# Optimization experiments

Hardware: AMD Instinct MI355X
Metric: run time of the kernel (lower is better)

The kernel has to match this reference:

```python
import jax, jax.numpy as jnp
import numpy as np

D = 1024      # input_dim / embed_dim
H = 1024      # hidden_dim
H2 = H // 2
M = 15        # n_masks
NH = 4        # n_heads
B = 8192
LN_EPS = 1e-5


def setup_inputs() -> dict:
    key = jax.random.key(0)
    ks = jax.random.split(key, 16)
    s = 0.02
    return {
        "x": jax.random.normal(ks[0], (B, D), jnp.float32),
        # nn.MultiheadAttention params (torch layout: y = x @ W.T + b)
        "in_proj_w": jax.random.normal(ks[1], (3 * D, D), jnp.float32) * s,
        "in_proj_b": jax.random.normal(ks[2], (3 * D,), jnp.float32) * s,
        "out_proj_w": jax.random.normal(ks[3], (D, D), jnp.float32) * s,
        "out_proj_b": jax.random.normal(ks[4], (D,), jnp.float32) * s,
        # 15 mask MLPs stacked along leading axis (grouped GEMM form)
        "W1": jax.random.normal(ks[5], (M, D, H), jnp.float32) * s,
        "b1": jax.random.normal(ks[6], (M, H), jnp.float32) * s,
        "ln_g": jnp.ones((M, H), jnp.float32),
        "ln_b": jnp.zeros((M, H), jnp.float32),
        "W2": jax.random.normal(ks[7], (M, H, H2), jnp.float32) * s,
        "b2": jax.random.normal(ks[8], (M, H2), jnp.float32) * s,
        "W3": jax.random.normal(ks[9], (M, H2, D), jnp.float32) * s,
        "b3": jax.random.normal(ks[10], (M, D), jnp.float32) * s,
    }


def reference(x, in_proj_w, in_proj_b, out_proj_w, out_proj_b,
              W1, b1, ln_g, ln_b, W2, b2, W3, b3):
    Bn = x.shape[0]
    hd = D // NH
    # --- seq_len=1 self-attention ---
    qkv = x @ in_proj_w.T + in_proj_b                      # [B, 3D]
    q, k, v = jnp.split(qkv, 3, axis=-1)                   # each [B, D]
    qh = q.reshape(Bn, NH, hd)
    kh = k.reshape(Bn, NH, hd)
    vh = v.reshape(Bn, NH, hd)
    scores = jnp.sum(qh * kh, axis=-1) / jnp.sqrt(jnp.float32(hd))  # [B, NH]
    # softmax over kv length = 1 -> all ones (kept for faithfulness)
    w = jax.nn.softmax(scores[..., None], axis=-1)         # [B, NH, 1]
    attn = (w * vh).reshape(Bn, D)                         # [B, D]
    a = attn @ out_proj_w.T + out_proj_b                   # [B, D]
    # --- 15 mask MLPs as one grouped GEMM stack (Dropout is eval->identity) ---
    h1 = jnp.einsum('bd,mdh->mbh', a, W1) + b1[:, None, :]  # [M, B, H]
    mu = jnp.mean(h1, axis=-1, keepdims=True)
    var = jnp.mean(jnp.square(h1 - mu), axis=-1, keepdims=True)
    h1 = (h1 - mu) * jax.lax.rsqrt(var + LN_EPS) * ln_g[:, None, :] + ln_b[:, None, :]
    h1 = jax.nn.gelu(h1, approximate=False)
    h2 = jnp.einsum('mbh,mhk->mbk', h1, W2) + b2[:, None, :]  # [M, B, H2]
    h2 = jax.nn.gelu(h2, approximate=False)
    h3 = jnp.einsum('mbk,mkd->mbd', h2, W3) + b3[:, None, :]  # [M, B, D]
    return jax.nn.sigmoid(h3)                               # [M, B, D]
```

## Files before the change

### kernel.cpp

```cpp
#include <hip/hip_runtime.h>

#define D_  1024
#define H_  1024
#define H2_ 512
#define M_  15
#define B_  8192

typedef __attribute__((ext_vector_type(4))) float f32x4;
typedef __attribute__((ext_vector_type(8))) short short8;

__device__ __forceinline__ unsigned short f2bf(float f) {
  unsigned int u = __float_as_uint(f);
  u += 0x7fffu + ((u >> 16) & 1u);
  return (unsigned short)(u >> 16);
}
__device__ __forceinline__ float bf2f(unsigned int h) {
  return __uint_as_float(h << 16);
}
__device__ __forceinline__ float gelu_exact(float x) {
  return 0.5f * x * (1.0f + erff(x * 0.70710678118654752440f));
}

__global__ void cast_f32_bf16(const float* __restrict__ in, unsigned short* __restrict__ out, int n4) {
  int i = blockIdx.x * blockDim.x + threadIdx.x;
  if (i >= n4) return;
  float4 v = ((const float4*)in)[i];
  ushort4 o;
  o.x = f2bf(v.x); o.y = f2bf(v.y); o.z = f2bf(v.z); o.w = f2bf(v.w);
  ((ushort4*)out)[i] = o;
}

__global__ void zero_f32(float* __restrict__ p, int n) {
  int i = blockIdx.x * blockDim.x + threadIdx.x;
  if (i < n) p[i] = 0.f;
}

__global__ void bias_fold(const float* __restrict__ opw, const float* __restrict__ bv,
                          const float* __restrict__ opb, float* __restrict__ bc) {
  const int o = blockIdx.x;
  const int l = threadIdx.x;
  float s = 0.f;
  for (int d = l; d < D_; d += 64) s += opw[(size_t)o * D_ + d] * bv[d];
#pragma unroll
  for (int off = 32; off > 0; off >>= 1) s += __shfl_down(s, off);
  if (l == 0) bc[o] = s + opb[o];
}

__global__ void transpose_cast(const float* __restrict__ in, unsigned short* __restrict__ out,
                               int K, int N) {
  __shared__ float t[32][33];
  const size_t mo = (size_t)blockIdx.z * K * N;
  in  += mo;
  out += mo;
  const int k0 = blockIdx.x * 32, n0 = blockIdx.y * 32;
  const int tx = threadIdx.x, ty = threadIdx.y;
#pragma unroll
  for (int j = 0; j < 32; j += 8)
    t[ty + j][tx] = in[(size_t)(k0 + ty + j) * N + (n0 + tx)];
  __syncthreads();
#pragma unroll
  for (int j = 0; j < 32; j += 8)
    out[(size_t)(n0 + ty + j) * K + (k0 + tx)] = f2bf(t[tx][ty + j]);
}

template <int EPI>
__launch_bounds__(256, 3)
__global__ void gemm_bt(const unsigned short* __restrict__ A, const unsigned short* __restrict__ Bt,
                        const float* __restrict__ bias, void* __restrict__ Cout,
                        int Mrows, int N, int K,
                        long sA, long sB, long sBias, long sC) {
  __shared__ __align__(16) unsigned short As[128 * 64];
  __shared__ __align__(16) unsigned short Bs[128 * 64];
  const int mz = blockIdx.z;
  A    += (size_t)mz * sA;
  Bt   += (size_t)mz * sB;
  bias += (size_t)mz * sBias;

  const int tid  = threadIdx.x;
  const int w    = tid >> 6;
  const int lane = tid & 63;
  const int row0 = blockIdx.x * 128;
  const int col0 = blockIdx.y * 128;

  f32x4 acc[4][4];
#pragma unroll
  for (int i = 0; i < 4; ++i)
#pragma unroll
    for (int j = 0; j < 4; ++j) acc[i][j] = (f32x4){0.f, 0.f, 0.f, 0.f};

  const int wm = w >> 1, wn = w & 1;
  const int mrow = lane & 15;
  const int kq   = (lane >> 4) << 3;

  for (int k0 = 0; k0 < K; k0 += 64) {
    __syncthreads();
#pragma unroll
    for (int i = 0; i < 4; ++i) {
      const int c  = i * 256 + tid;
      const int m  = c >> 3;
      const int kk = (c & 7) << 3;
      const unsigned short* gA = A  + (size_t)(row0 + m) * K + (k0 + kk);
      const unsigned short* gB = Bt + (size_t)(col0 + m) * K + (k0 + kk);
      const int ldsoff = (i * 256 + w * 64) * 8;
      __builtin_amdgcn_global_load_lds((const __attribute__((address_space(1))) void*)gA,
                                       (__attribute__((address_space(3))) void*)(As + ldsoff),
                                       16, 0, 0);
      __builtin_amdgcn_global_load_lds((const __attribute__((address_space(1))) void*)gB,
                                       (__attribute__((address_space(3))) void*)(Bs + ldsoff),
                                       16, 0, 0);
    }
    __syncthreads();
#pragma unroll
    for (int ki = 0; ki < 64; ki += 32) {
      short8 af[4], bf[4];
#pragma unroll
      for (int f = 0; f < 4; ++f) {
        af[f] = *(const short8*)(As + (wm * 64 + f * 16 + mrow) * 64 + ki + kq);
        bf[f] = *(const short8*)(Bs + (wn * 64 + f * 16 + mrow) * 64 + ki + kq);
      }
#pragma unroll
      for (int fm = 0; fm < 4; ++fm)
#pragma unroll
        for (int fn = 0; fn < 4; ++fn)
          acc[fm][fn] = __builtin_amdgcn_mfma_f32_16x16x32_bf16(af[fm], bf[fn], acc[fm][fn], 0, 0, 0);
    }
  }

  float*          Cf = (float*)Cout          + (size_t)mz * sC;
  unsigned short* Cb = (unsigned short*)Cout + (size_t)mz * sC;
  const int rq = (lane >> 4) << 2;
  const int cl = lane & 15;
#pragma unroll
  for (int fm = 0; fm < 4; ++fm) {
#pragma unroll
    for (int fn = 0; fn < 4; ++fn) {
      const int cc = col0 + wn * 64 + fn * 16 + cl;
      const float bv = bias[cc];
#pragma unroll
      for (int r = 0; r < 4; ++r) {
        const int rr = row0 + wm * 64 + fm * 16 + rq + r;
        float v = acc[fm][fn][r] + bv;
        if (EPI == 2) {
          Cf[(size_t)rr * N + cc] = 1.0f / (1.0f + __expf(-v));
        } else {
          if (EPI == 1) v = gelu_exact(v);
          Cb[(size_t)rr * N + cc] = f2bf(v);
        }
      }
    }
  }
}

#define BAR()   asm volatile("s_barrier" ::: "memory")
#define LGKM0() asm volatile("s_waitcnt lgkmcnt(0)" ::: "memory")
#define VM6()   asm volatile("s_waitcnt vmcnt(6)" ::: "memory")

#define STG_A(bufi, bA, rho0) do {                                                             \
  _Pragma("unroll")                                                                            \
  for (int j_ = 0; j_ < 2; ++j_) {                                                             \
    const int rho_ = (rho0) + j_ * 64 + (tid >> 3);                                            \
    const int gr_  = (((rho_ >> 6) & 1) << 7) | (((rho_ >> 7) & 1) << 6) | (rho_ & 63);        \
    const unsigned short* g_ = (bA) + (size_t)gr_ * K + (((tid & 7) ^ (rho_ & 7)) << 3);       \
    __builtin_amdgcn_global_load_lds((const __attribute__((address_space(1))) void*)g_,        \
        (__attribute__((address_space(3))) void*)(&As[bufi][(rho0) * 64 + (j_ * 512 + w6 * 64) * 8]), \
        16, 0, 0);                                                                             \
  }                                                                                            \
} while (0)

#define STG_B(bufi, bB, rho0) do {                                                             \
  _Pragma("unroll")                                                                            \
  for (int j_ = 0; j_ < 2; ++j_) {                                                             \
    const int rho_ = (rho0) + j_ * 64 + (tid >> 3);                                            \
    const int gc_  = (((rho_ >> 5) & 3) << 6) | (((rho_ >> 7) & 1) << 5) | (rho_ & 31);        \
    const unsigned short* g_ = (bB) + (size_t)gc_ * K + (((tid & 7) ^ (rho_ & 7)) << 3);       \
    __builtin_amdgcn_global_load_lds((const __attribute__((address_space(1))) void*)g_,        \
        (__attribute__((address_space(3))) void*)(&Bs[bufi][(rho0) * 64 + (j_ * 512 + w6 * 64) * 8]), \
        16, 0, 0);                                                                             \
  }                                                                                            \
} while (0)

#define LDA4(bufi, hi) do {                                                                    \
  _Pragma("unroll")                                                                            \
  for (int q_ = 0; q_ < 4; ++q_) {                                                             \
    const int rho_ = ((hi) ? 128 : 0) + wm * 64 + q_ * 16 + lrow;                              \
    a[q_][0] = *(const short8*)&As[bufi][rho_ * 64 + ((lk ^ (rho_ & 7)) << 3)];                \
    a[q_][1] = *(const short8*)&As[bufi][rho_ * 64 + (((4 + lk) ^ (rho_ & 7)) << 3)];          \
  }                                                                                            \
} while (0)

#define LDB2(bufi, hi) do {                                                                    \
  _Pragma("unroll")                                                                            \
  for (int q_ = 0; q_ < 2; ++q_) {                                                             \
    const int rho_ = ((hi) ? 128 : 0) + wn * 32 + q_ * 16 + lrow;                              \
    b[(hi) * 2 + q_][0] = *(const short8*)&Bs[bufi][rho_ * 64 + ((lk ^ (rho_ & 7)) << 3)];     \
    b[(hi) * 2 + q_][1] = *(const short8*)&Bs[bufi][rho_ * 64 + (((4 + lk) ^ (rho_ & 7)) << 3)]; \
  }                                                                                            \
} while (0)

#define MMQ(mh, nh) do {                                                                       \
  __builtin_amdgcn_s_setprio(1);                                                               \
  _Pragma("unroll")                                                                            \
  for (int mq_ = 0; mq_ < 4; ++mq_) {                                                          \
    _Pragma("unroll")                                                                          \
    for (int nq_ = 0; nq_ < 2; ++nq_) {                                                        \
      acc[(mh) * 4 + mq_][(nh) * 2 + nq_] = __builtin_amdgcn_mfma_f32_16x16x32_bf16(           \
          a[mq_][0], b[(nh) * 2 + nq_][0], acc[(mh) * 4 + mq_][(nh) * 2 + nq_], 0, 0, 0);      \
      acc[(mh) * 4 + mq_][(nh) * 2 + nq_] = __builtin_amdgcn_mfma_f32_16x16x32_bf16(           \
          a[mq_][1], b[(nh) * 2 + nq_][1], acc[(mh) * 4 + mq_][(nh) * 2 + nq_], 0, 0, 0);      \
    }                                                                                          \
  }                                                                                            \
  __builtin_amdgcn_s_setprio(0);                                                               \
} while (0)

template <int EPI, int LNT, int LGY>
__launch_bounds__(512, 2)
__global__ void gemm256p(const unsigned short* __restrict__ A, const unsigned short* __restrict__ Bt,
                         const float* __restrict__ bias, void* __restrict__ Cout,
                         int N, int K, long sA, long sB, long sBias, long sC,
                         int ntiles8, int tpb) {
  __shared__ __align__(16) unsigned short As[2][256 * 64];
  __shared__ __align__(16) unsigned short Bs[2][256 * 64];
  const int NT = 1 << LNT, GYm1 = (1 << LGY) - 1;

  const int bid = blockIdx.x;
  const int xcd = bid & 7, lb = bid >> 3;
  const int cb  = xcd * ntiles8;

  const int tid  = threadIdx.x;
  const int w6   = tid >> 6;
  const int lane = tid & 63;
  const int wm   = w6 >> 2;
  const int wn   = w6 & 3;
  const int lrow = lane & 15;
  const int lk   = lane >> 4;

  int t_cur = 0;
  int tix  = cb + lb;
  int row0 = ((tix >> LGY) & 31) << 8;
  int col0 = (tix & GYm1) << 8;
  int mz   = tix >> (LGY + 5);
  const unsigned short* bAc = A  + (size_t)mz * sA + (size_t)row0 * K;
  const unsigned short* bBc = Bt + (size_t)mz * sB + (size_t)col0 * K;

  f32x4 acc[8][4];
#pragma unroll
  for (int i = 0; i < 8; ++i)
#pragma unroll
    for (int j = 0; j < 4; ++j) acc[i][j] = (f32x4){0.f, 0.f, 0.f, 0.f};
  short8 a[4][2], b[4][2];

  STG_A(0, bAc, 0); STG_B(0, bBc, 0); STG_B(0, bBc, 128); STG_A(0, bAc, 128);
  STG_A(1, bAc + 64, 0); STG_B(1, bBc + 64, 0); STG_B(1, bBc + 64, 128);
  VM6(); BAR();

  const int totK = tpb << LNT;
#pragma unroll 1
  for (int T = 0; T < totK; T += 2) {
    const int g2 = (T + 2 < totK) ? T + 2 : totK - 1;
    const int g3 = (T + 3 < totK) ? T + 3 : totK - 1;
    const int t2 = g2 >> LNT, t3 = g3 >> LNT;
    const int tix2 = cb + lb + t2 * 30;
    const int tix3 = cb + lb + t3 * 30;
    const unsigned short* bA2 = A  + (size_t)(tix2 >> (LGY + 5)) * sA
                                   + (size_t)((((tix2 >> LGY) & 31) << 8)) * K + ((g2 & (NT - 1)) << 6);
    const unsigned short* bB2 = Bt + (size_t)(tix2 >> (LGY + 5)) * sB
                                   + (size_t)(((tix2 & GYm1) << 8)) * K + ((g2 & (NT - 1)) << 6);
    const unsigned short* bA3 = A  + (size_t)(tix3 >> (LGY + 5)) * sA
                                   + (size_t)((((tix3 >> LGY) & 31) << 8)) * K + ((g3 & (NT - 1)) << 6);
    const unsigned short* bB3 = Bt + (size_t)(tix3 >> (LGY + 5)) * sB
                                   + (size_t)(((tix3 & GYm1) << 8)) * K + ((g3 & (NT - 1)) << 6);
    const unsigned short* bA1 = bAc + (((T + 1) & (NT - 1)) << 6);

    LDA4(0, 0); LDB2(0, 0); LDB2(0, 1);
    STG_A(1, bA1, 128);
    BAR(); LGKM0();
    MMQ(0, 0); MMQ(0, 1);
    BAR();
    LDA4(0, 1);
    STG_A(0, bA2, 0); STG_B(0, bB2, 0); STG_B(0, bB2, 128);
    VM6(); BAR(); LGKM0();
    MMQ(1, 0); MMQ(1, 1);
    BAR();
    LDA4(1, 0); LDB2(1, 0); LDB2(1, 1);
    STG_A(0, bA2, 128);
    BAR(); LGKM0();
    MMQ(0, 0); MMQ(0, 1);
    BAR();
    LDA4(1, 1);
    STG_A(1, bA3, 0); STG_B(1, bB3, 0); STG_B(1, bB3, 128);
    VM6(); BAR(); LGKM0();
    MMQ(1, 0); MMQ(1, 1);
    BAR();

    if (((T + 2) & (NT - 1)) == 0) {
      const float* bp = bias + (size_t)mz * sBias;
      float*          Cf = (float*)Cout          + (size_t)mz * sC;
      unsigned short* Cb = (unsigned short*)Cout + (size_t)mz * sC;
      const int rq = (lane >> 4) << 2;
      const int cl = lane & 15;
#pragma unroll
      for (int nf = 0; nf < 4; ++nf) {
        const int cc = col0 + wn * 64 + nf * 16 + cl;
        const float bv = bp[cc];
#pragma unroll
        for (int mf = 0; mf < 8; ++mf) {
#pragma unroll
          for (int r = 0; r < 4; ++r) {
            const int rr = row0 + wm * 128 + mf * 16 + rq + r;
            float v = acc[mf][nf][r] + bv;
            if (EPI == 2) {
              Cf[(size_t)rr * N + cc] = 1.0f / (1.0f + __expf(-v));
            } else {
              if (EPI == 1) v = gelu_exact(v);
              Cb[(size_t)rr * N + cc] = f2bf(v);
            }
          }
        }
      }
#pragma unroll
      for (int i = 0; i < 8; ++i)
#pragma unroll
        for (int j = 0; j < 4; ++j) acc[i][j] = (f32x4){0.f, 0.f, 0.f, 0.f};
      ++t_cur;
      if (t_cur < tpb) {
        tix  = cb + lb + t_cur * 30;
        row0 = ((tix >> LGY) & 31) << 8;
        col0 = (tix & GYm1) << 8;
        mz   = tix >> (LGY + 5);
        bAc  = A  + (size_t)mz * sA + (size_t)row0 * K;
        bBc  = Bt + (size_t)mz * sB + (size_t)col0 * K;
      }
    }
  }
  asm volatile("s_waitcnt vmcnt(0)" ::: "memory");
}

__global__ void ln_gelu(const unsigned short* __restrict__ in, const float* __restrict__ g,
                        const float* __restrict__ bb, unsigned short* __restrict__ out) {
  const int m = blockIdx.y;
  in  += (size_t)m * B_ * H_;
  out += (size_t)m * B_ * H_;
  g   += (size_t)m * H_;
  bb  += (size_t)m * H_;
  const int row = blockIdx.x;
  const int tid = threadIdx.x;
  const unsigned short* rp = in + (size_t)row * H_;
  uint2 u = ((const uint2*)rp)[tid];
  float x0 = bf2f(u.x & 0xffffu);
  float x1 = bf2f(u.x >> 16);
  float x2 = bf2f(u.y & 0xffffu);
  float x3 = bf2f(u.y >> 16);

  float s  = x0 + x1 + x2 + x3;
  float s2 = x0 * x0 + x1 * x1 + x2 * x2 + x3 * x3;
#pragma unroll
  for (int o = 32; o > 0; o >>= 1) {
    s  += __shfl_down(s, o);
    s2 += __shfl_down(s2, o);
  }
  __shared__ float red[10];
  const int w = tid >> 6;
  if ((tid & 63) == 0) { red[w] = s; red[4 + w] = s2; }
  __syncthreads();
  if (tid == 0) {
    float ts = red[0] + red[1] + red[2] + red[3];
    float t2 = red[4] + red[5] + red[6] + red[7];
    float mean = ts * (1.0f / H_);
    float var  = t2 * (1.0f / H_) - mean * mean;
    red[8] = mean;
    red[9] = rsqrtf(var + 1e-5f);
  }
  __syncthreads();
  const float mean = red[8], rstd = red[9];
  const int col = tid * 4;
  float y0 = gelu_exact((x0 - mean) * rstd * g[col + 0] + bb[col + 0]);
  float y1 = gelu_exact((x1 - mean) * rstd * g[col + 1] + bb[col + 1]);
  float y2 = gelu_exact((x2 - mean) * rstd * g[col + 2] + bb[col + 2]);
  float y3 = gelu_exact((x3 - mean) * rstd * g[col + 3] + bb[col + 3]);
  ushort4 o;
  o.x = f2bf(y0); o.y = f2bf(y1); o.z = f2bf(y2); o.w = f2bf(y3);
  ((ushort4*)(out + (size_t)row * H_))[tid] = o;
}

extern "C" void kernel_launch(void* const* d_in, const int* in_sizes, int n_in,
                              void* d_out, int out_size, void* d_ws, size_t ws_size,
                              hipStream_t stream) {
  const float* x   = (const float*)d_in[0];
  const float* ipw = (const float*)d_in[1];
  const float* ipb = (const float*)d_in[2];
  const float* opw = (const float*)d_in[3];
  const float* opb = (const float*)d_in[4];
  const float* W1  = (const float*)d_in[5];
  const float* b1  = (const float*)d_in[6];
  const float* lng = (const float*)d_in[7];
  const float* lnb = (const float*)d_in[8];
  const float* W2  = (const float*)d_in[9];
  const float* b2  = (const float*)d_in[10];
  const float* W3  = (const float*)d_in[11];
  const float* b3  = (const float*)d_in[12];
  float* out = (float*)d_out;

  char* p = (char*)d_ws;
  auto take = [&](size_t bytes) { void* q = (void*)p; p += (bytes + 255) & ~(size_t)255; return q; };
  unsigned short* xb  = (unsigned short*)take((size_t)B_ * D_ * 2);
  unsigned short* wob = (unsigned short*)take((size_t)D_ * D_ * 2);
  unsigned short* wvt = (unsigned short*)take((size_t)D_ * D_ * 2);
  unsigned short* wcb = (unsigned short*)take((size_t)D_ * D_ * 2);
  float*          zb  = (float*)take((size_t)D_ * 4);
  float*          bc  = (float*)take((size_t)D_ * 4);
  unsigned short* w1t = (unsigned short*)take((size_t)M_ * H_ * D_ * 2);
  unsigned short* w2t = (unsigned short*)take((size_t)M_ * H2_ * H_ * 2);
  unsigned short* w3t = (unsigned short*)take((size_t)M_ * D_ * H2_ * 2);
  unsigned short* ab  = (unsigned short*)take((size_t)B_ * D_ * 2);
  unsigned short* h1p = (unsigned short*)take((size_t)M_ * B_ * H_ * 2);
  unsigned short* h1a = (unsigned short*)take((size_t)M_ * B_ * H_ * 2);
  unsigned short* h2b = (unsigned short*)take((size_t)M_ * B_ * H2_ * 2);

  cast_f32_bf16<<<dim3((B_ * D_ / 4 + 255) / 256), 256, 0, stream>>>(x, xb, B_ * D_ / 4);
  cast_f32_bf16<<<dim3((D_ * D_ / 4 + 255) / 256), 256, 0, stream>>>(opw, wob, D_ * D_ / 4);
  transpose_cast<<<dim3(D_ / 32, D_ / 32, 1), dim3(32, 8), 0, stream>>>(ipw + 2 * D_ * D_, wvt, D_, D_);
  transpose_cast<<<dim3(D_ / 32, H_ / 32, M_), dim3(32, 8), 0, stream>>>(W1, w1t, D_, H_);
  transpose_cast<<<dim3(H_ / 32, H2_ / 32, M_), dim3(32, 8), 0, stream>>>(W2, w2t, H_, H2_);
  transpose_cast<<<dim3(H2_ / 32, D_ / 32, M_), dim3(32, 8), 0, stream>>>(W3, w3t, H2_, D_);
  zero_f32<<<dim3(4), 256, 0, stream>>>(zb, D_);

  gemm_bt<0><<<dim3(D_ / 128, D_ / 128, 1), 256, 0, stream>>>(
      wob, wvt, zb, wcb, D_, D_, D_, 0, 0, 0, 0);
  bias_fold<<<dim3(D_), 64, 0, stream>>>(opw, ipb + 2 * D_, opb, bc);
  gemm_bt<0><<<dim3(B_ / 128, D_ / 128, 1), 256, 0, stream>>>(
      xb, wcb, bc, ab, B_, D_, D_, 0, 0, 0, 0);

  gemm256p<0, 4, 2><<<dim3(240), 512, 0, stream>>>(
      ab, w1t, b1, h1p, H_, D_,
      0, (long)H_ * D_, (long)H_, (long)B_ * H_, 1920 / 8, 8);
  ln_gelu<<<dim3(B_, M_), 256, 0, stream>>>(h1p, lng, lnb, h1a);
  gemm256p<1, 4, 1><<<dim3(240), 512, 0, stream>>>(
      h1a, w2t, b2, h2b, H2_, H_,
      (long)B_ * H_, (long)H2_ * H_, (long)H2_, (long)B_ * H2_, 960 / 8, 4);
  gemm256p<2, 3, 2><<<dim3(240), 512, 0, stream>>>(
      h2b, w3t, b3, out, D_, H2_,
      (long)B_ * H2_, (long)D_ * H2_, (long)D_, (long)B_ * D_, 1920 / 8, 8);
}
```

Before: 1.666 ms.

## Fuse first MLP GEMM with LayerNorm and GELU epilogue using full-row tiles

```diff
diff --git a/kernel.cpp b/kernel.cpp
--- a/kernel.cpp
+++ b/kernel.cpp
@@ -154,6 +154,149 @@
 #define BAR()   asm volatile("s_barrier" ::: "memory")
 #define LGKM0() asm volatile("s_waitcnt lgkmcnt(0)" ::: "memory")
 #define VM6()   asm volatile("s_waitcnt vmcnt(6)" ::: "memory")
+
+#define STGLN(gp_) do {                                                                        \
+  int gg_ = (gp_); if (gg_ > 255) gg_ = 254;       \
+  const int tp_ = gg_ >> 5, kp_ = gg_ & 31, bi_ = gg_ & 1;                                     \
+  const int tixp_ = cb + tp_ * 30 + lb;                                                        \
+  const int mp_ = tixp_ >> 7, r0p_ = (tixp_ & 127) << 6;                                       \
+  const unsigned short* Ab_ = A + (size_t)r0p_ * D_ + kp_ * 32;                                \
+  const unsigned short* Bb_ = Bt + (size_t)mp_ * (H_ * D_) + kp_ * 32;                         \
+  _Pragma("unroll")                                                                            \
+  for (int l_ = 0; l_ < 8; ++l_) {                                                             \
+    const int fl_ = l_ * 512 + tid;                                                            \
+    __builtin_amdgcn_global_load_lds(                                                          \
+        (const __attribute__((address_space(1))) void*)(Bb_ + (size_t)(fl_ >> 2) * D_ + (fl_ & 3) * 8), \
+        (__attribute__((address_space(3))) void*)(&Bsb[bi_][fl_ * 8]), 16, 0, 0);              \
+  }                                                                                            \
+  if (w6 < 4) {                                                                                \
+    __builtin_amdgcn_global_load_lds(                                                          \
+        (const __attribute__((address_space(1))) void*)(Ab_ + (size_t)(tid >> 2) * D_ + (tid & 3) * 8), \
+        (__attribute__((address_space(3))) void*)(&Asb[bi_][tid * 8]), 16, 0, 0);              \
+  }                                                                                            \
+} while (0)
+
+__launch_bounds__(512, 2)
+__global__ void gemm_ln(const unsigned short* __restrict__ A,
+                        const unsigned short* __restrict__ Bt,
+                        const float* __restrict__ b1, const float* __restrict__ lng,
+                        const float* __restrict__ lnb, unsigned short* __restrict__ out) {
+  __shared__ __align__(16) unsigned short Asb[2][64 * 32];
+  __shared__ __align__(16) unsigned short Bsb[2][1024 * 32];
+
+  const int bid = blockIdx.x;
+  const int xcd = bid & 7, lb = bid >> 3;
+  const int cb  = xcd * 240;
+
+  const int tid  = threadIdx.x;
+  const int w6   = tid >> 6;
+  const int lane = tid & 63;
+  const int cl   = lane & 15;
+  const int rq   = (lane >> 4) << 2;
+  const int kq8  = (lane >> 4) << 3;
+
+  f32x4 acc[4][8];
+#pragma unroll
+  for (int i = 0; i < 4; ++i)
+#pragma unroll
+    for (int j = 0; j < 8; ++j) acc[i][j] = (f32x4){0.f, 0.f, 0.f, 0.f};
+
+  STGLN(0);
+#pragma unroll 1
+  for (int g = 0; g < 256; ++g) {
+    STGLN(g + 1);
+    if (w6 < 4) { asm volatile("s_waitcnt vmcnt(9)" ::: "memory"); }
+    else        { asm volatile("s_waitcnt vmcnt(8)" ::: "memory"); }
+    BAR();
+    {
+      const int bi = g & 1;
+      short8 af[4], bfv[8];
+#pragma unroll
+      for (int mf = 0; mf < 4; ++mf)
+        af[mf] = *(const short8*)&Asb[bi][(mf * 16 + cl) * 32 + kq8];
+#pragma unroll
+      for (int nf = 0; nf < 8; ++nf)
+        bfv[nf] = *(const short8*)&Bsb[bi][(w6 * 128 + nf * 16 + cl) * 32 + kq8];
+#pragma unroll
+      for (int nf = 0; nf < 8; ++nf)
+#pragma unroll
+        for (int mf = 0; mf < 4; ++mf)
+          acc[mf][nf] = __builtin_amdgcn_mfma_f32_16x16x32_bf16(af[mf], bfv[nf], acc[mf][nf], 0, 0, 0);
+    }
+    BAR();
+    if ((g & 31) == 31) {
+      const int tc   = g >> 5;
+      const int tixc = cb + tc * 30 + lb;
+      const int mc   = tixc >> 7;
+      const int r0   = (tixc & 127) << 6;
+      const float* b1p = b1 + (size_t)mc * H_;
+      const float* gp  = lng + (size_t)mc * H_;
+      const float* bp  = lnb + (size_t)mc * H_;
+      float b1v[8], gv[8], bv[8];
+#pragma unroll
+      for (int nf = 0; nf < 8; ++nf) {
+        const int col = w6 * 128 + nf * 16 + cl;
+        b1v[nf] = b1p[col]; gv[nf] = gp[col]; bv[nf] = bp[col];
+      }
+      float* pS = (float*)&Bsb[1][0];
+      float* pQ = pS + 64 * 8;
+      float* st = pQ + 64 * 8;
+#pragma unroll
+      for (int mf = 0; mf < 4; ++mf)
+#pragma unroll
+        for (int r = 0; r < 4; ++r) {
+          float s = 0.f, s2 = 0.f;
+#pragma unroll
+          for (int nf = 0; nf < 8; ++nf) {
+            float v = acc[mf][nf][r] + b1v[nf];
+            acc[mf][nf][r] = v;
+            s += v; s2 += v * v;
+          }
+#pragma unroll
+          for (int d = 1; d < 16; d <<= 1) {
+            s  += __shfl_xor(s, d);
+            s2 += __shfl_xor(s2, d);
+          }
+          if (cl == 0) {
+            const int row = mf * 16 + rq + r;
+            pS[row * 8 + w6] = s;
+            pQ[row * 8 + w6] = s2;
+          }
+        }
+      BAR();
+      if (tid < 64) {
+        float ts = 0.f, t2 = 0.f;
+#pragma unroll
+        for (int j = 0; j < 8; ++j) { ts += pS[tid * 8 + j]; t2 += pQ[tid * 8 + j]; }
+        const float mean = ts * (1.0f / H_);
+        const float var  = t2 * (1.0f / H_) - mean * mean;
+        st[tid * 2]     = mean;
+        st[tid * 2 + 1] = rsqrtf(var + 1e-5f);
+      }
+      BAR();
+#pragma unroll
+      for (int mf = 0; mf < 4; ++mf)
+#pragma unroll
+        for (int r = 0; r < 4; ++r) {
+          const int row = mf * 16 + rq + r;
+          const float mean = st[row * 2], rstd = st[row * 2 + 1];
+          unsigned short* op = out + ((size_t)mc * B_ + r0 + row) * H_;
+#pragma unroll
+          for (int nf = 0; nf < 8; ++nf) {
+            const int col = w6 * 128 + nf * 16 + cl;
+            const float y = gelu_exact((acc[mf][nf][r] - mean) * rstd * gv[nf] + bv[nf]);
+            op[col] = f2bf(y);
+          }
+        }
+#pragma unroll
+      for (int i = 0; i < 4; ++i)
+#pragma unroll
+        for (int j = 0; j < 8; ++j) acc[i][j] = (f32x4){0.f, 0.f, 0.f, 0.f};
+      BAR();
+    }
+  }
+  asm volatile("s_waitcnt vmcnt(0)" ::: "memory");
+}
 
 #define STG_A(bufi, bA, rho0) do {                                                             \
   _Pragma("unroll")                                                                            \
@@ -335,53 +478,6 @@
   asm volatile("s_waitcnt vmcnt(0)" ::: "memory");
 }
 
-__global__ void ln_gelu(const unsigned short* __restrict__ in, const float* __restrict__ g,
-                        const float* __restrict__ bb, unsigned short* __restrict__ out) {
-  const int m = blockIdx.y;
-  in  += (size_t)m * B_ * H_;
-  out += (size_t)m * B_ * H_;
-  g   += (size_t)m * H_;
-  bb  += (size_t)m * H_;
-  const int row = blockIdx.x;
-  const int tid = threadIdx.x;
-  const unsigned short* rp = in + (size_t)row * H_;
-  uint2 u = ((const uint2*)rp)[tid];
-  float x0 = bf2f(u.x & 0xffffu);
-  float x1 = bf2f(u.x >> 16);
-  float x2 = bf2f(u.y & 0xffffu);
-  float x3 = bf2f(u.y >> 16);
-
-  float s  = x0 + x1 + x2 + x3;
-  float s2 = x0 * x0 + x1 * x1 + x2 * x2 + x3 * x3;
-#pragma unroll
-  for (int o = 32; o > 0; o >>= 1) {
-    s  += __shfl_down(s, o);
-    s2 += __shfl_down(s2, o);
-  }
-  __shared__ float red[10];
-  const int w = tid >> 6;
-  if ((tid & 63) == 0) { red[w] = s; red[4 + w] = s2; }
-  __syncthreads();
-  if (tid == 0) {
-    float ts = red[0] + red[1] + red[2] + red[3];
-    float t2 = red[4] + red[5] + red[6] + red[7];
-    float mean = ts * (1.0f / H_);
-    float var  = t2 * (1.0f / H_) - mean * mean;
-    red[8] = mean;
-    red[9] = rsqrtf(var + 1e-5f);
-  }
-  __syncthreads();
-  const float mean = red[8], rstd = red[9];
-  const int col = tid * 4;
-  float y0 = gelu_exact((x0 - mean) * rstd * g[col + 0] + bb[col + 0]);
-  float y1 = gelu_exact((x1 - mean) * rstd * g[col + 1] + bb[col + 1]);
-  float y2 = gelu_exact((x2 - mean) * rstd * g[col + 2] + bb[col + 2]);
-  float y3 = gelu_exact((x3 - mean) * rstd * g[col + 3] + bb[col + 3]);
-  ushort4 o;
-  o.x = f2bf(y0); o.y = f2bf(y1); o.z = f2bf(y2); o.w = f2bf(y3);
-  ((ushort4*)(out + (size_t)row * H_))[tid] = o;
-}
-
 extern "C" void kernel_launch(void* const* d_in, const int* in_sizes, int n_in,
                               void* d_out, int out_size, void* d_ws, size_t ws_size,
                               hipStream_t stream) {
@@ -412,7 +508,6 @@
   unsigned short* w2t = (unsigned short*)take((size_t)M_ * H2_ * H_ * 2);
   unsigned short* w3t = (unsigned short*)take((size_t)M_ * D_ * H2_ * 2);
   unsigned short* ab  = (unsigned short*)take((size_t)B_ * D_ * 2);
-  unsigned short* h1p = (unsigned short*)take((size_t)M_ * B_ * H_ * 2);
   unsigned short* h1a = (unsigned short*)take((size_t)M_ * B_ * H_ * 2);
   unsigned short* h2b = (unsigned short*)take((size_t)M_ * B_ * H2_ * 2);
 
@@ -430,10 +525,8 @@
   gemm_bt<0><<<dim3(B_ / 128, D_ / 128, 1), 256, 0, stream>>>(
       xb, wcb, bc, ab, B_, D_, D_, 0, 0, 0, 0);
 
-  gemm256p<0, 4, 2><<<dim3(240), 512, 0, stream>>>(
-      ab, w1t, b1, h1p, H_, D_,
-      0, (long)H_ * D_, (long)H_, (long)B_ * H_, 1920 / 8, 8);
-  ln_gelu<<<dim3(B_, M_), 256, 0, stream>>>(h1p, lng, lnb, h1a);
+  gemm_ln<<<dim3(240), 512, 0, stream>>>(ab, w1t, b1, lng, lnb, h1a);
+
   gemm256p<1, 4, 1><<<dim3(240), 512, 0, stream>>>(
       h1a, w2t, b2, h2b, H2_, H_,
       (long)B_ * H_, (long)H2_ * H_, (long)H2_, (long)B_ * H2_, 960 / 8, 4);
```

Result: slower. 1.796 ms (+7.8%).
